# Kernel tuning notes

Hardware: AMD Instinct MI355X
Metric: run time of the kernel (lower is better)

Reference implementation:

```python
import jax, jax.numpy as jnp
import numpy as np

EPS = 1e-5  # BatchNorm2d default eps; running stats at init: mean=0, var=1


def conv_bn_silu(x, w, gamma, beta):
    # 1x1 conv (no bias) + BatchNorm (mean=0, var=1) + SiLU
    y = jnp.einsum('bchw,oc->bohw', x, w)
    y = y * (gamma / jnp.sqrt(1.0 + EPS))[None, :, None, None] + beta[None, :, None, None]
    return jax.nn.silu(y)


def setup_inputs() -> dict:
    key = jax.random.key(0)
    ks = jax.random.split(key, 13)
    c1, c2 = 256, 256
    ci = c2 // 8   # 32  (theta/phi)
    cg = c2 // 2   # 128 (g)
    b, h, w = 8, 56, 56
    sd = lambda cin: 1.0 / np.sqrt(cin)
    return {
        'x':       jax.random.normal(ks[0], (b, c1, h, w), jnp.float32),
        'w_theta': jax.random.normal(ks[1], (ci, c1), jnp.float32) * sd(c1),
        'g_theta': jnp.ones((ci,), jnp.float32),
        'b_theta': jnp.zeros((ci,), jnp.float32),
        'w_phi':   jax.random.normal(ks[2], (ci, c1), jnp.float32) * sd(c1),
        'g_phi':   jnp.ones((ci,), jnp.float32),
        'b_phi':   jnp.zeros((ci,), jnp.float32),
        'w_g':     jax.random.normal(ks[3], (cg, c1), jnp.float32) * sd(c1),
        'g_g':     jnp.ones((cg,), jnp.float32),
        'b_g':     jnp.zeros((cg,), jnp.float32),
        'w_out':   jax.random.normal(ks[4], (c2, cg), jnp.float32) * sd(cg),
        'g_out':   jnp.ones((c2,), jnp.float32),
        'b_out':   jnp.zeros((c2,), jnp.float32),
    }


def reference(x, w_theta, g_theta, b_theta, w_phi, g_phi, b_phi,
              w_g, g_g, b_g, w_out, g_out, b_out):
    b, c, h, w = x.shape
    hw = h * w
    theta = conv_bn_silu(x, w_theta, g_theta, b_theta).reshape(b, -1, hw).transpose(0, 2, 1)  # [b,hw,ci]
    phi   = conv_bn_silu(x, w_phi,   g_phi,   b_phi).reshape(b, -1, hw)                       # [b,ci,hw]
    g     = conv_bn_silu(x, w_g,     g_g,     b_g).reshape(b, -1, hw).transpose(0, 2, 1)      # [b,hw,cg]
    attn = jax.nn.softmax(jnp.einsum('bnc,bcm->bnm', theta, phi), axis=-1)                    # [b,hw,hw]
    out = jnp.einsum('bnm,bmc->bnc', attn, g).transpose(0, 2, 1).reshape(b, -1, h, w)         # [b,cg,h,w]
    return conv_bn_silu(out, w_out, g_out, b_out) + x
```

## Files before the change

kernel.cpp:

```cpp
#include <hip/hip_runtime.h>

typedef __bf16 bf16;
typedef __bf16 bf16x4 __attribute__((ext_vector_type(4)));
typedef __bf16 bf16x8 __attribute__((ext_vector_type(8)));
typedef float f32x4 __attribute__((ext_vector_type(4)));

#define MFMA16(a,b,c) __builtin_amdgcn_mfma_f32_16x16x32_bf16((a),(b),(c),0,0,0)

__device__ __forceinline__ float silu_f(float y){ return y/(1.f+__expf(-y)); }

__device__ __forceinline__ bf16x8 ld8f(const float* __restrict__ p){
    float4 a = *(const float4*)p;
    float4 b = *(const float4*)(p+4);
    bf16x8 r;
    r[0]=(bf16)a.x; r[1]=(bf16)a.y; r[2]=(bf16)a.z; r[3]=(bf16)a.w;
    r[4]=(bf16)b.x; r[5]=(bf16)b.y; r[6]=(bf16)b.z; r[7]=(bf16)b.w;
    return r;
}

#define BN_SCALE 0.9999950000374997f

__global__ __launch_bounds__(256) void qkv_kernel(
    const float* __restrict__ xg,
    const float* __restrict__ wth, const float* __restrict__ gth, const float* __restrict__ bth,
    const float* __restrict__ wph, const float* __restrict__ gph, const float* __restrict__ bph,
    const float* __restrict__ wgg, const float* __restrict__ ggg, const float* __restrict__ bgg,
    bf16* __restrict__ Qb, bf16* __restrict__ Kb, bf16* __restrict__ Vtb)
{
    const int b = blockIdx.x, pt = blockIdx.y;
    const int p0 = pt*64;
    const int t = threadIdx.x;
    const int lane = t & 63, wv = t >> 6;
    const int lc = lane & 15, lg = lane >> 4;

    __shared__ __align__(16) bf16 xT[64][264];

    {
        const int cbase = t >> 4;
        const int p4 = (t & 15) * 4;
        #pragma unroll
        for (int r = 0; r < 16; ++r) {
            int c = r*16 + cbase;
            float4 v = *(const float4*)(xg + ((size_t)(b*256 + c))*3136 + p0 + p4);
            xT[p4+0][c] = (bf16)v.x; xT[p4+1][c] = (bf16)v.y;
            xT[p4+2][c] = (bf16)v.z; xT[p4+3][c] = (bf16)v.w;
        }
    }
    __syncthreads();

    const f32x4 fz = {0.f,0.f,0.f,0.f};

    for (int tt = 0; tt < 3; ++tt) {
        const int ot = wv*3 + tt;
        if (ot < 4) {
            const float *W, *gam, *bet; bf16* dst; int ol;
            if (ot < 2) { W=wth; gam=gth; bet=bth; dst=Qb; ol=ot*16; }
            else        { W=wph; gam=gph; bet=bph; dst=Kb; ol=(ot-2)*16; }
            f32x4 acc[4]; acc[0]=fz; acc[1]=fz; acc[2]=fz; acc[3]=fz;
            #pragma unroll
            for (int ks = 0; ks < 8; ++ks) {
                bf16x8 wf = ld8f(W + (size_t)(ol+lc)*256 + ks*32 + lg*8);
                #pragma unroll
                for (int pf = 0; pf < 4; ++pf) {
                    bf16x8 af = *(const bf16x8*)&xT[pf*16+lc][ks*32+lg*8];
                    acc[pf] = MFMA16(af, wf, acc[pf]);
                }
            }
            const int oc = ol + lc;
            const float sc = gam[oc] * BN_SCALE;
            const float bi = bet[oc];
            #pragma unroll
            for (int pf = 0; pf < 4; ++pf)
                #pragma unroll
                for (int r = 0; r < 4; ++r) {
                    int pos = p0 + pf*16 + lg*4 + r;
                    dst[((size_t)b*3136 + pos)*32 + oc] = (bf16)silu_f(acc[pf][r]*sc + bi);
                }
        } else {
            const int ol = (ot-4)*16;
            f32x4 acc[4]; acc[0]=fz; acc[1]=fz; acc[2]=fz; acc[3]=fz;
            #pragma unroll
            for (int ks = 0; ks < 8; ++ks) {
                bf16x8 wf = ld8f(wgg + (size_t)(ol+lc)*256 + ks*32 + lg*8);
                #pragma unroll
                for (int pc = 0; pc < 4; ++pc) {
                    bf16x8 xf = *(const bf16x8*)&xT[pc*16+lc][ks*32+lg*8];
                    acc[pc] = MFMA16(wf, xf, acc[pc]);
                }
            }
            #pragma unroll
            for (int r = 0; r < 4; ++r) {
                const int oc = ol + lg*4 + r;
                const float sc = ggg[oc] * BN_SCALE;
                const float bi = bgg[oc];
                #pragma unroll
                for (int pc = 0; pc < 4; ++pc) {
                    int pos = p0 + pc*16 + lc;
                    Vtb[((size_t)b*128 + oc)*3136 + pos] = (bf16)silu_f(acc[pc][r]*sc + bi);
                }
            }
        }
    }
}

__global__ __launch_bounds__(256) void attn_kernel(
    const bf16* __restrict__ Qb, const bf16* __restrict__ Kb,
    const bf16* __restrict__ Vtb, bf16* __restrict__ Ob)
{
    const int b = blockIdx.x, qt = blockIdx.y;
    const int p0 = qt*64;
    const int t = threadIdx.x;
    const int lane = t & 63, wv = t >> 6;
    const int lc = lane & 15, lg = lane >> 4;

    __shared__ __align__(16) bf16 Klds[64][40];
    __shared__ __align__(16) bf16 Vlds[128][72];
    __shared__ __align__(16) bf16 Plds[4][16][72];

    const bf16* Kbase = Kb + (size_t)b*3136*32;
    const bf16* Vbase = Vtb + (size_t)b*128*3136;

    bf16x8 qf = *(const bf16x8*)(Qb + ((size_t)b*3136 + p0 + wv*16 + lc)*32 + lg*8);

    float mrow[4] = {-1e30f,-1e30f,-1e30f,-1e30f};
    float lrow[4] = {0.f,0.f,0.f,0.f};
    const f32x4 fz = {0.f,0.f,0.f,0.f};
    f32x4 oacc[8];
    #pragma unroll
    for (int cf = 0; cf < 8; ++cf) oacc[cf] = fz;

    const int krow = t >> 2, kkp = (t & 3) * 8;
    const int vc   = t >> 3, vkp = (t & 7) * 8;

    for (int kt = 0; kt < 49; ++kt) {
        const int k0 = kt*64;
        __syncthreads();
        *(bf16x8*)&Klds[krow][kkp] = *(const bf16x8*)(Kbase + (size_t)(k0+krow)*32 + kkp);
        #pragma unroll
        for (int r = 0; r < 4; ++r) {
            int c = r*32 + vc;
            *(bf16x8*)&Vlds[c][vkp] = *(const bf16x8*)(Vbase + (size_t)c*3136 + k0 + vkp);
        }
        __syncthreads();

        f32x4 s[4];
        #pragma unroll
        for (int nf = 0; nf < 4; ++nf) {
            bf16x8 kf = *(const bf16x8*)&Klds[nf*16+lc][lg*8];
            s[nf] = MFMA16(qf, kf, fz);
        }

        float scale[4];
        #pragma unroll
        for (int r = 0; r < 4; ++r) {
            float mx = fmaxf(fmaxf(s[0][r], s[1][r]), fmaxf(s[2][r], s[3][r]));
            #pragma unroll
            for (int d = 1; d < 16; d <<= 1) mx = fmaxf(mx, __shfl_xor(mx, d));
            float nm = fmaxf(mrow[r], mx);
            float sc = __expf(mrow[r] - nm);
            float ps = 0.f;
            #pragma unroll
            for (int nf = 0; nf < 4; ++nf) { float pv = __expf(s[nf][r]-nm); s[nf][r]=pv; ps+=pv; }
            #pragma unroll
            for (int d = 1; d < 16; d <<= 1) ps += __shfl_xor(ps, d);
            lrow[r] = lrow[r]*sc + ps;
            mrow[r] = nm;
            scale[r] = sc;
        }
        #pragma unroll
        for (int cf = 0; cf < 8; ++cf)
            #pragma unroll
            for (int r = 0; r < 4; ++r) oacc[cf][r] *= scale[r];

        #pragma unroll
        for (int nf = 0; nf < 4; ++nf)
            #pragma unroll
            for (int r = 0; r < 4; ++r)
                Plds[wv][lg*4+r][nf*16+lc] = (bf16)s[nf][r];

        #pragma unroll
        for (int ks = 0; ks < 2; ++ks) {
            bf16x8 pfr = *(const bf16x8*)&Plds[wv][lc][ks*32 + lg*8];
            #pragma unroll
            for (int cf = 0; cf < 8; ++cf) {
                bf16x8 vf = *(const bf16x8*)&Vlds[cf*16+lc][ks*32+lg*8];
                oacc[cf] = MFMA16(pfr, vf, oacc[cf]);
            }
        }
    }

    #pragma unroll
    for (int cf = 0; cf < 8; ++cf)
        #pragma unroll
        for (int r = 0; r < 4; ++r) {
            int q = p0 + wv*16 + lg*4 + r;
            Ob[((size_t)b*3136 + q)*128 + cf*16 + lc] = (bf16)(oacc[cf][r] / lrow[r]);
        }
}

__global__ __launch_bounds__(256) void out_kernel(
    const bf16* __restrict__ Ob, const float* __restrict__ wout,
    const float* __restrict__ gout, const float* __restrict__ bout,
    const float* __restrict__ xg, float* __restrict__ outp)
{
    const int b = blockIdx.x, pt = blockIdx.y;
    const int p0 = pt*64;
    const int t = threadIdx.x;
    const int lane = t & 63, wv = t >> 6;
    const int lc = lane & 15, lg = lane >> 4;

    __shared__ __align__(16) bf16 Olds[64][136];
    __shared__ __align__(16) bf16 outlds[4][64][72];

    {
        const int row = t >> 2;
        const int cb = (t & 3) * 32;
        #pragma unroll
        for (int r = 0; r < 4; ++r) {
            int cp = cb + r*8;
            *(bf16x8*)&Olds[row][cp] = *(const bf16x8*)(Ob + ((size_t)b*3136 + p0 + row)*128 + cp);
        }
    }
    __syncthreads();

    const f32x4 fz = {0.f,0.f,0.f,0.f};
    f32x4 acc[4][4];
    #pragma unroll
    for (int pf = 0; pf < 4; ++pf)
        #pragma unroll
        for (int nf = 0; nf < 4; ++nf) acc[pf][nf] = fz;

    #pragma unroll
    for (int ks = 0; ks < 4; ++ks) {
        bf16x8 wf[4];
        #pragma unroll
        for (int nf = 0; nf < 4; ++nf)
            wf[nf] = ld8f(wout + (size_t)(wv*64 + nf*16 + lc)*128 + ks*32 + lg*8);
        #pragma unroll
        for (int pf = 0; pf < 4; ++pf) {
            bf16x8 af = *(const bf16x8*)&Olds[pf*16+lc][ks*32+lg*8];
            #pragma unroll
            for (int nf = 0; nf < 4; ++nf)
                acc[pf][nf] = MFMA16(af, wf[nf], acc[pf][nf]);
        }
    }

    #pragma unroll
    for (int nf = 0; nf < 4; ++nf) {
        const int oc = wv*64 + nf*16 + lc;
        const float sc = gout[oc] * BN_SCALE;
        const float bi = bout[oc];
        #pragma unroll
        for (int pf = 0; pf < 4; ++pf)
            #pragma unroll
            for (int r = 0; r < 4; ++r)
                outlds[wv][nf*16+lc][pf*16+lg*4+r] = (bf16)silu_f(acc[pf][nf][r]*sc + bi);
    }

    #pragma unroll
    for (int i = 0; i < 16; ++i) {
        const int orow = i*4 + lg;
        const int oc = wv*64 + orow;
        const int p4 = lc*4;
        bf16x4 vo = *(const bf16x4*)&outlds[wv][orow][p4];
        float4 vx = *(const float4*)(xg + ((size_t)b*256 + oc)*3136 + p0 + p4);
        float4 res;
        res.x = (float)vo[0] + vx.x;
        res.y = (float)vo[1] + vx.y;
        res.z = (float)vo[2] + vx.z;
        res.w = (float)vo[3] + vx.w;
        *(float4*)(outp + ((size_t)b*256 + oc)*3136 + p0 + p4) = res;
    }
}

extern "C" void kernel_launch(void* const* d_in, const int* in_sizes, int n_in,
                              void* d_out, int out_size, void* d_ws, size_t ws_size,
                              hipStream_t stream)
{
    const float* x    = (const float*)d_in[0];
    const float* wth  = (const float*)d_in[1];
    const float* gth  = (const float*)d_in[2];
    const float* bth  = (const float*)d_in[3];
    const float* wph  = (const float*)d_in[4];
    const float* gph  = (const float*)d_in[5];
    const float* bph  = (const float*)d_in[6];
    const float* wgg  = (const float*)d_in[7];
    const float* ggg  = (const float*)d_in[8];
    const float* bgg  = (const float*)d_in[9];
    const float* wout = (const float*)d_in[10];
    const float* gout = (const float*)d_in[11];
    const float* bout = (const float*)d_in[12];

    bf16* ws  = (bf16*)d_ws;
    bf16* Qb  = ws;
    bf16* Kb  = Qb + (size_t)8*3136*32;
    bf16* Vtb = Kb + (size_t)8*3136*32;
    bf16* Ob  = Vtb + (size_t)8*128*3136;

    dim3 grid(8, 49), blk(256);
    qkv_kernel<<<grid, blk, 0, stream>>>(x, wth, gth, bth, wph, gph, bph,
                                         wgg, ggg, bgg, Qb, Kb, Vtb);
    attn_kernel<<<grid, blk, 0, stream>>>(Qb, Kb, Vtb, Ob);
    out_kernel<<<grid, blk, 0, stream>>>(Ob, wout, gout, bout, x, (float*)d_out);
}
```

Before: 236.0 us.

## Split attention over key chunks with combine kernel, lazy rescale, swizzled P tile

Splits the key dimension of the flash-attention kernel into four chunks across a third grid dimension, so the grid goes from 392 blocks to 1568 and fills more compute units. Partial unnormalized outputs plus per-row max and sum are written to workspace, and a new combine kernel merges them with log-sum-exp weights. It also skips the running-max rescale of the accumulators unless the new max exceeds the old by more than 8, and XOR-swizzles the P tile in LDS to cut bank conflicts. The cost is extra global traffic for the partials, one more kernel launch, and bf16 rounding of unnormalized partial outputs.

```diff
diff --git a/kernel.cpp b/kernel.cpp
--- a/kernel.cpp
+++ b/kernel.cpp
@@ -105,9 +105,12 @@
 
 __global__ __launch_bounds__(256) void attn_kernel(
     const bf16* __restrict__ Qb, const bf16* __restrict__ Kb,
-    const bf16* __restrict__ Vtb, bf16* __restrict__ Ob)
-{
-    const int b = blockIdx.x, qt = blockIdx.y;
+    const bf16* __restrict__ Vtb, bf16* __restrict__ Opart,
+    float* __restrict__ mpart, float* __restrict__ lpart)
+{
+    const int b = blockIdx.x, qt = blockIdx.y, z = blockIdx.z;
+    const int kt0 = (z==0) ? 0  : 13 + 12*(z-1);
+    const int kt1 = (z==3) ? 49 : 13 + 12*z;
     const int p0 = qt*64;
     const int t = threadIdx.x;
     const int lane = t & 63, wv = t >> 6;
@@ -115,7 +118,7 @@
 
     __shared__ __align__(16) bf16 Klds[64][40];
     __shared__ __align__(16) bf16 Vlds[128][72];
-    __shared__ __align__(16) bf16 Plds[4][16][72];
+    __shared__ __align__(16) bf16 Plds[4][16*72];
 
     const bf16* Kbase = Kb + (size_t)b*3136*32;
     const bf16* Vbase = Vtb + (size_t)b*128*3136;
@@ -131,8 +134,10 @@
 
     const int krow = t >> 2, kkp = (t & 3) * 8;
     const int vc   = t >> 3, vkp = (t & 7) * 8;
-
-    for (int kt = 0; kt < 49; ++kt) {
+    const int pxorw = (lg >> 1) << 4;
+    const int pxorr = (lc >> 3) << 4;
+
+    for (int kt = kt0; kt < kt1; ++kt) {
         const int k0 = kt*64;
         __syncthreads();
         *(bf16x8*)&Klds[krow][kkp] = *(const bf16x8*)(Kbase + (size_t)(k0+krow)*32 + kkp);
@@ -150,37 +155,51 @@
             s[nf] = MFMA16(qf, kf, fz);
         }
 
-        float scale[4];
-        #pragma unroll
-        for (int r = 0; r < 4; ++r) {
-            float mx = fmaxf(fmaxf(s[0][r], s[1][r]), fmaxf(s[2][r], s[3][r]));
-            #pragma unroll
-            for (int d = 1; d < 16; d <<= 1) mx = fmaxf(mx, __shfl_xor(mx, d));
-            float nm = fmaxf(mrow[r], mx);
-            float sc = __expf(mrow[r] - nm);
+        float mx[4];
+        #pragma unroll
+        for (int r = 0; r < 4; ++r) {
+            float m = fmaxf(fmaxf(s[0][r], s[1][r]), fmaxf(s[2][r], s[3][r]));
+            #pragma unroll
+            for (int d = 1; d < 16; d <<= 1) m = fmaxf(m, __shfl_xor(m, d));
+            mx[r] = m;
+        }
+        bool ok = (mx[0] <= mrow[0]+8.f) && (mx[1] <= mrow[1]+8.f)
+               && (mx[2] <= mrow[2]+8.f) && (mx[3] <= mrow[3]+8.f);
+        if (!__all(ok)) {
+            float scale[4];
+            #pragma unroll
+            for (int r = 0; r < 4; ++r) {
+                float nm = fmaxf(mrow[r], mx[r]);
+                scale[r] = __expf(mrow[r] - nm);
+                mrow[r] = nm;
+                lrow[r] *= scale[r];
+            }
+            #pragma unroll
+            for (int cf = 0; cf < 8; ++cf)
+                #pragma unroll
+                for (int r = 0; r < 4; ++r) oacc[cf][r] *= scale[r];
+        }
+        #pragma unroll
+        for (int r = 0; r < 4; ++r) {
             float ps = 0.f;
             #pragma unroll
-            for (int nf = 0; nf < 4; ++nf) { float pv = __expf(s[nf][r]-nm); s[nf][r]=pv; ps+=pv; }
+            for (int nf = 0; nf < 4; ++nf) {
+                float pv = __expf(s[nf][r] - mrow[r]); s[nf][r] = pv; ps += pv;
+            }
             #pragma unroll
             for (int d = 1; d < 16; d <<= 1) ps += __shfl_xor(ps, d);
-            lrow[r] = lrow[r]*sc + ps;
-            mrow[r] = nm;
-            scale[r] = sc;
-        }
-        #pragma unroll
-        for (int cf = 0; cf < 8; ++cf)
-            #pragma unroll
-            for (int r = 0; r < 4; ++r) oacc[cf][r] *= scale[r];
+            lrow[r] += ps;
+        }
 
         #pragma unroll
         for (int nf = 0; nf < 4; ++nf)
             #pragma unroll
             for (int r = 0; r < 4; ++r)
-                Plds[wv][lg*4+r][nf*16+lc] = (bf16)s[nf][r];
+                Plds[wv][(lg*4+r)*72 + ((nf*16+lc) ^ pxorw)] = (bf16)s[nf][r];
 
         #pragma unroll
         for (int ks = 0; ks < 2; ++ks) {
-            bf16x8 pfr = *(const bf16x8*)&Plds[wv][lc][ks*32 + lg*8];
+            bf16x8 pfr = *(const bf16x8*)&Plds[wv][lc*72 + ((ks*32 + lg*8) ^ pxorr)];
             #pragma unroll
             for (int cf = 0; cf < 8; ++cf) {
                 bf16x8 vf = *(const bf16x8*)&Vlds[cf*16+lc][ks*32+lg*8];
@@ -194,8 +213,54 @@
         #pragma unroll
         for (int r = 0; r < 4; ++r) {
             int q = p0 + wv*16 + lg*4 + r;
-            Ob[((size_t)b*3136 + q)*128 + cf*16 + lc] = (bf16)(oacc[cf][r] / lrow[r]);
-        }
+            Opart[((size_t)(z*8+b)*3136 + q)*128 + cf*16 + lc] = (bf16)oacc[cf][r];
+        }
+    if (lc == 0) {
+        #pragma unroll
+        for (int r = 0; r < 4; ++r) {
+            int q = p0 + wv*16 + lg*4 + r;
+            size_t idx = (size_t)(z*8+b)*3136 + q;
+            mpart[idx] = mrow[r];
+            lpart[idx] = lrow[r];
+        }
+    }
+}
+
+__global__ __launch_bounds__(256) void combine_kernel(
+    const bf16* __restrict__ Opart, const float* __restrict__ mpart,
+    const float* __restrict__ lpart, bf16* __restrict__ Ob)
+{
+    const int b = blockIdx.x, qt = blockIdx.y;
+    const int t = threadIdx.x;
+    #pragma unroll
+    for (int it = 0; it < 4; ++it) {
+        int gi = it*256 + t;
+        int q = qt*64 + (gi >> 4);
+        int c8 = (gi & 15) * 8;
+        float m0 = mpart[(size_t)(0*8+b)*3136 + q];
+        float m1 = mpart[(size_t)(1*8+b)*3136 + q];
+        float m2 = mpart[(size_t)(2*8+b)*3136 + q];
+        float m3 = mpart[(size_t)(3*8+b)*3136 + q];
+        float M = fmaxf(fmaxf(m0,m1), fmaxf(m2,m3));
+        float w0 = __expf(m0-M), w1 = __expf(m1-M), w2 = __expf(m2-M), w3 = __expf(m3-M);
+        float L = lpart[(size_t)(0*8+b)*3136 + q]*w0 + lpart[(size_t)(1*8+b)*3136 + q]*w1
+                + lpart[(size_t)(2*8+b)*3136 + q]*w2 + lpart[(size_t)(3*8+b)*3136 + q]*w3;
+        float inv = 1.f / L;
+        float o[8];
+        #pragma unroll
+        for (int j = 0; j < 8; ++j) o[j] = 0.f;
+        #pragma unroll
+        for (int zz = 0; zz < 4; ++zz) {
+            float w = (zz==0)?w0:(zz==1)?w1:(zz==2)?w2:w3;
+            bf16x8 v = *(const bf16x8*)(Opart + ((size_t)(zz*8+b)*3136 + q)*128 + c8);
+            #pragma unroll
+            for (int j = 0; j < 8; ++j) o[j] += w * (float)v[j];
+        }
+        bf16x8 rr;
+        #pragma unroll
+        for (int j = 0; j < 8; ++j) rr[j] = (bf16)(o[j]*inv);
+        *(bf16x8*)(Ob + ((size_t)b*3136 + q)*128 + c8) = rr;
+    }
 }
 
 __global__ __launch_bounds__(256) void out_kernel(
@@ -292,14 +357,18 @@
     const float* bout = (const float*)d_in[12];
 
     bf16* ws  = (bf16*)d_ws;
-    bf16* Qb  = ws;
-    bf16* Kb  = Qb + (size_t)8*3136*32;
-    bf16* Vtb = Kb + (size_t)8*3136*32;
-    bf16* Ob  = Vtb + (size_t)8*128*3136;
-
-    dim3 grid(8, 49), blk(256);
-    qkv_kernel<<<grid, blk, 0, stream>>>(x, wth, gth, bth, wph, gph, bph,
-                                         wgg, ggg, bgg, Qb, Kb, Vtb);
-    attn_kernel<<<grid, blk, 0, stream>>>(Qb, Kb, Vtb, Ob);
-    out_kernel<<<grid, blk, 0, stream>>>(Ob, wout, gout, bout, x, (float*)d_out);
-}
+    bf16* Qb    = ws;
+    bf16* Kb    = Qb + (size_t)8*3136*32;
+    bf16* Vtb   = Kb + (size_t)8*3136*32;
+    bf16* Ob    = Vtb + (size_t)8*128*3136;
+    bf16* Opart = Ob + (size_t)8*3136*128;
+    float* mpart = (float*)(Opart + (size_t)4*8*3136*128);
+    float* lpart = mpart + (size_t)4*8*3136;
+
+    dim3 blk(256);
+    qkv_kernel<<<dim3(8,49), blk, 0, stream>>>(x, wth, gth, bth, wph, gph, bph,
+                                               wgg, ggg, bgg, Qb, Kb, Vtb);
+    attn_kernel<<<dim3(8,49,4), blk, 0, stream>>>(Qb, Kb, Vtb, Opart, mpart, lpart);
+    combine_kernel<<<dim3(8,49), blk, 0, stream>>>(Opart, mpart, lpart, Ob);
+    out_kernel<<<dim3(8,49), blk, 0, stream>>>(Ob, wout, gout, bout, x, (float*)d_out);
+}
```

New measurement: 221.3 us. 1.07x faster.
